# Kernel tuning notes

Hardware: AMD Instinct MI355X
Metric: run time of the kernel (lower is better)

Reference implementation:

```python
import jax, jax.numpy as jnp
import numpy as np
import math

NUM_HEADS = 8

def _ln(x, g, b, eps=1e-5):
    mu = x.mean(-1, keepdims=True)
    var = ((x - mu) ** 2).mean(-1, keepdims=True)
    return (x - mu) / jnp.sqrt(var + eps) * g + b

def setup_inputs() -> dict:
    key = jax.random.key(0)
    ks = jax.random.split(key, 10)
    B, Nq, Nk, dQ, dK, dV = 16, 1024, 1024, 512, 512, 512
    s = 0.05  # small init so the double-exp in masked_softmax stays finite
    Q = jax.random.normal(ks[0], (B, Nq, dQ), jnp.float32)
    K = jax.random.normal(ks[1], (B, Nk, dK), jnp.float32)
    Qm = (jax.random.uniform(ks[2], (B, Nq, 1)) < 0.9).astype(jnp.float32)
    Km = (jax.random.uniform(ks[3], (B, Nk, 1)) < 0.9).astype(jnp.float32)
    Wq = jax.random.normal(ks[4], (dQ, dV), jnp.float32) * s
    Wk = jax.random.normal(ks[5], (dK, dV), jnp.float32) * s
    Wv = jax.random.normal(ks[6], (dK, dV), jnp.float32) * s
    Wo = jax.random.normal(ks[7], (dV, dV), jnp.float32) * s
    bq = jnp.zeros((dV,), jnp.float32); bk = jnp.zeros((dV,), jnp.float32)
    bv = jnp.zeros((dV,), jnp.float32); bo = jnp.zeros((dV,), jnp.float32)
    g0 = jnp.ones((dV,), jnp.float32); b0 = jnp.zeros((dV,), jnp.float32)
    g1 = jnp.ones((dV,), jnp.float32); b1 = jnp.zeros((dV,), jnp.float32)
    return {"Q": Q, "K": K, "Qm": Qm, "Km": Km,
            "Wq": Wq, "bq": bq, "Wk": Wk, "bk": bk, "Wv": Wv, "bv": bv,
            "Wo": Wo, "bo": bo, "g0": g0, "b0": b0, "g1": g1, "b1": b1}

def reference(Q, K, Qm, Km, Wq, bq, Wk, bk, Wv, bv, Wo, bo, g0, b0, g1, b1):
    B, Nq, _ = Q.shape
    Nk = K.shape[1]
    dV = Wq.shape[1]
    h = NUM_HEADS
    dh = dV // h
    # projections + feature masking (Qm/Km broadcast over feature dim)
    Qp = (Q @ Wq + bq) * Qm          # [B,Nq,dV]
    Kp = (K @ Wk + bk) * Km          # [B,Nk,dV]
    V  = K @ Wv + bv                 # [B,Nk,dV]
    # head split: torch.cat(split(dh,2),0) == head-major [h,B,N,dh]
    Qh = Qp.reshape(B, Nq, h, dh).transpose(2, 0, 1, 3)
    Kh = Kp.reshape(B, Nk, h, dh).transpose(2, 0, 1, 3)
    Vh = V.reshape(B, Nk, h, dh).transpose(2, 0, 1, 3)
    S = jnp.einsum('hbqd,hbkd->hbqk', Qh, Kh) / math.sqrt(dV)
    # faithful masked_softmax: exp applied twice (Km branch then Qm branch)
    X = jnp.exp(S) * Km[:, :, 0][None, :, None, :]   # [h,B,Nq,Nk]
    X = jnp.exp(X) * Qm[:, :, 0][None, :, :, None]
    A = X / (X.sum(-1, keepdims=True) + 1e-8)
    O = Qh + jnp.einsum('hbqk,hbkd->hbqd', A, Vh)    # residual in head space
    O = O.transpose(1, 2, 0, 3).reshape(B, Nq, dV)   # merge heads back
    O = _ln(O, g0, b0)
    O = O + jax.nn.relu(O @ Wo + bo)
    return _ln(O, g1, b1)
```

## Files before the change

### kernel.cpp

```cpp
#include <hip/hip_runtime.h>
#include <hip/hip_bf16.h>
#include <cstdint>


typedef __bf16 bf16;
typedef __bf16 bf16x4 __attribute__((ext_vector_type(4)));
typedef __bf16 bf16x8 __attribute__((ext_vector_type(8)));
typedef float f32x4 __attribute__((ext_vector_type(4)));

#define MFMA16(a, b, c) __builtin_amdgcn_mfma_f32_16x16x32_bf16((a), (b), (c), 0, 0, 0)

#if __has_builtin(__builtin_amdgcn_exp2f)
#define EXP2F(x) __builtin_amdgcn_exp2f(x)
#else
#define EXP2F(x) exp2f(x)
#endif

static __device__ __forceinline__ void async_lds16(const bf16* g, bf16* l) {
  __builtin_amdgcn_global_load_lds(
      (__attribute__((address_space(1))) void*)(void*)g,
      (__attribute__((address_space(3))) void*)l,
      16, 0, 0);
}

static __device__ __forceinline__ void swz512(int id, long& rowBase, int& colBase) {
  colBase = ((id >> 3) & 3) * 128;
  rowBase = (long)((id & 7) + 8 * (id >> 5)) * 128;
}

struct ConvArgs {
  const float* src[10];
  bf16* dst[10];
  int n[10];
};

__global__ __launch_bounds__(256) void prep(
    const float* __restrict__ Wq, const float* __restrict__ Wk,
    const float* __restrict__ Wv, const float* __restrict__ Wo,
    bf16* __restrict__ Tq, bf16* __restrict__ Tk,
    bf16* __restrict__ Tv, bf16* __restrict__ To, ConvArgs ca) {
  __shared__ bf16 t[64][72];
  const int id = blockIdx.x;
  const int tid = threadIdx.x;
  if (id < 256) {
    const int bx = id & 7, by = (id >> 3) & 7, bz = id >> 6;
    const float* src;
    bf16* dst;
    switch (bz) {
      case 0: src = Wq; dst = Tq; break;
      case 1: src = Wk; dst = Tk; break;
      case 2: src = Wv; dst = Tv; break;
      default: src = Wo; dst = To; break;
    }
    const int n0 = bx * 64;
    const int k0 = by * 64;
    for (int c = tid; c < 512; c += 256) {
      const int row = c >> 3, col = (c & 7) * 8;
      const float* sp = src + (size_t)(k0 + row) * 512 + n0 + col;
      const f32x4 a = *(const f32x4*)sp;
      const f32x4 b = *(const f32x4*)(sp + 4);
      bf16x8 v;
#pragma unroll
      for (int j = 0; j < 4; ++j) { v[j] = (bf16)a[j]; v[j + 4] = (bf16)b[j]; }
      *(bf16x8*)(&t[row][col]) = v;
    }
    __syncthreads();
    for (int c = tid; c < 512; c += 256) {
      const int row = c >> 3, col8 = (c & 7) * 8;
      bf16x8 v;
#pragma unroll
      for (int j = 0; j < 8; ++j) v[j] = t[col8 + j][row];
      *(bf16x8*)(dst + (size_t)(n0 + row) * 512 + k0 + col8) = v;
    }
  } else {
    const int cid = id - 256;
    const int seg = cid >> 3;
    const int n = ca.n[seg];
    const long i = ((long)(cid & 7) * 256 + tid) * 8;
    if (i >= n) return;
    const float* s = ca.src[seg];
    const f32x4 x0 = *(const f32x4*)(s + i);
    const f32x4 x1 = *(const f32x4*)(s + i + 4);
    bf16x8 o;
#pragma unroll
    for (int j = 0; j < 4; ++j) { o[j] = (bf16)x0[j]; o[j + 4] = (bf16)x1[j]; }
    *(bf16x8*)(ca.dst[seg] + i) = o;
  }
}

__global__ __launch_bounds__(256, 2) void gemm512(
    const bf16* __restrict__ A, const bf16* __restrict__ Bt,
    const bf16* __restrict__ bias, const bf16* __restrict__ mask,
    const bf16* __restrict__ resid, bf16* __restrict__ out) {
  __shared__ bf16 sA[128 * 32];
  __shared__ bf16 sB[128 * 32];
  const int tid = threadIdx.x;
  const int lane = tid & 63;
  const int w = tid >> 6;
  const int fm = lane & 15;
  const int fq = lane >> 4;
  long rowBase; int colBase;
  swz512(blockIdx.x, rowBase, colBase);

  f32x4 acc[4][4] = {};

  const int c0 = tid, c1 = tid + 256;
  const int r0 = c0 >> 2, o0 = (c0 & 3) * 8;
  const int r1 = c1 >> 2, o1 = (c1 & 3) * 8;
  const bf16* A0 = A + (rowBase + r0) * 512 + o0;
  const bf16* A1 = A + (rowBase + r1) * 512 + o1;
  const bf16* B0 = Bt + (size_t)(colBase + r0) * 512 + o0;
  const bf16* B1 = Bt + (size_t)(colBase + r1) * 512 + o1;

  const int wr = (w & 1) * 64;
  const int wc = (w >> 1) * 64;

  for (int kt = 0; kt < 16; ++kt) {
    const int k0 = kt * 32;
    __syncthreads();
    async_lds16(A0 + k0, sA + c0 * 8);
    async_lds16(A1 + k0, sA + c1 * 8);
    async_lds16(B0 + k0, sB + c0 * 8);
    async_lds16(B1 + k0, sB + c1 * 8);
    __syncthreads();
    bf16x8 a[4], b[4];
#pragma unroll
    for (int i = 0; i < 4; ++i)
      a[i] = *(const bf16x8*)(sA + (wr + i * 16 + fm) * 32 + fq * 8);
#pragma unroll
    for (int j = 0; j < 4; ++j)
      b[j] = *(const bf16x8*)(sB + (wc + j * 16 + fm) * 32 + fq * 8);
#pragma unroll
    for (int i = 0; i < 4; ++i)
#pragma unroll
      for (int j = 0; j < 4; ++j)
        acc[i][j] = MFMA16(a[i], b[j], acc[i][j]);
  }

#pragma unroll
  for (int i = 0; i < 4; ++i) {
#pragma unroll
    for (int r = 0; r < 4; ++r) {
      const long R = rowBase + wr + i * 16 + fq * 4 + r;
      const float mk = mask ? (float)mask[R] : 1.0f;
      const bf16* resrow = resid ? resid + R * 512 : nullptr;
      bf16* outrow = out + R * 512;
#pragma unroll
      for (int j = 0; j < 4; ++j) {
        const int C = colBase + wc + j * 16 + fm;
        float v = acc[i][j][r] + (float)bias[C];
        if (mask) v *= mk;
        if (resid) v = (float)resrow[C] + fmaxf(v, 0.0f);
        outrow[C] = (bf16)v;
      }
    }
  }
}

__global__ __launch_bounds__(256, 2) void proj_all(
    const float* __restrict__ Qf, const float* __restrict__ Kf,
    const bf16* __restrict__ Tq, const bf16* __restrict__ Tk,
    const bf16* __restrict__ Tv, const bf16* __restrict__ bq,
    const bf16* __restrict__ bk, const bf16* __restrict__ bv,
    const bf16* __restrict__ Qm, const bf16* __restrict__ Km,
    bf16* __restrict__ Qp, bf16* __restrict__ Kp, bf16* __restrict__ Vt) {
  __shared__ bf16 sA[128 * 32];
  __shared__ bf16 sB1[128 * 32];
  __shared__ bf16 sB2[128 * 32];
  const int tid = threadIdx.x;
  const int lane = tid & 63;
  const int w = tid >> 6;
  const int fm = lane & 15;
  const int fq = lane >> 4;
  const int wr = (w & 1) * 64;
  const int wc = (w >> 1) * 64;
  const int c0 = tid, c1 = tid + 256;
  const int r0 = c0 >> 2, o0 = (c0 & 3) * 8;
  const int r1 = c1 >> 2, o1 = (c1 & 3) * 8;

  if (blockIdx.x < 512) {
    long rowBase; int colBase;
    swz512(blockIdx.x, rowBase, colBase);
    f32x4 acc[4][4] = {};
    const float* A0 = Qf + (rowBase + r0) * 512 + o0;
    const float* A1 = Qf + (rowBase + r1) * 512 + o1;
    const bf16* B0 = Tq + (size_t)(colBase + r0) * 512 + o0;
    const bf16* B1 = Tq + (size_t)(colBase + r1) * 512 + o1;

    f32x4 x0 = *(const f32x4*)(A0);
    f32x4 x1 = *(const f32x4*)(A0 + 4);
    f32x4 y0 = *(const f32x4*)(A1);
    f32x4 y1 = *(const f32x4*)(A1 + 4);

    for (int kt = 0; kt < 16; ++kt) {
      __syncthreads();
      async_lds16(B0 + kt * 32, sB1 + c0 * 8);
      async_lds16(B1 + kt * 32, sB1 + c1 * 8);
      {
        bf16x8 va, vb;
#pragma unroll
        for (int j = 0; j < 4; ++j) {
          va[j] = (bf16)x0[j]; va[j + 4] = (bf16)x1[j];
          vb[j] = (bf16)y0[j]; vb[j + 4] = (bf16)y1[j];
        }
        *(bf16x8*)(sA + c0 * 8) = va;
        *(bf16x8*)(sA + c1 * 8) = vb;
      }
      __syncthreads();
      if (kt < 15) {
        const int k1 = kt * 32 + 32;
        x0 = *(const f32x4*)(A0 + k1);
        x1 = *(const f32x4*)(A0 + k1 + 4);
        y0 = *(const f32x4*)(A1 + k1);
        y1 = *(const f32x4*)(A1 + k1 + 4);
      }
      bf16x8 a[4], b[4];
#pragma unroll
      for (int i = 0; i < 4; ++i)
        a[i] = *(const bf16x8*)(sA + (wr + i * 16 + fm) * 32 + fq * 8);
#pragma unroll
      for (int j = 0; j < 4; ++j)
        b[j] = *(const bf16x8*)(sB1 + (wc + j * 16 + fm) * 32 + fq * 8);
#pragma unroll
      for (int i = 0; i < 4; ++i)
#pragma unroll
        for (int j = 0; j < 4; ++j)
          acc[i][j] = MFMA16(a[i], b[j], acc[i][j]);
    }

#pragma unroll
    for (int i = 0; i < 4; ++i) {
#pragma unroll
      for (int r = 0; r < 4; ++r) {
        const long R = rowBase + wr + i * 16 + fq * 4 + r;
        const float mk = (float)Qm[R];
        bf16* outrow = Qp + R * 512;
#pragma unroll
        for (int j = 0; j < 4; ++j) {
          const int C = colBase + wc + j * 16 + fm;
          outrow[C] = (bf16)((acc[i][j][r] + (float)bq[C]) * mk);
        }
      }
    }
  } else {
    long rowBase; int colBase;
    swz512(blockIdx.x - 512, rowBase, colBase);
    f32x4 acck[4][4] = {};
    f32x4 accv[4][4] = {};
    const float* A0 = Kf + (rowBase + r0) * 512 + o0;
    const float* A1 = Kf + (rowBase + r1) * 512 + o1;
    const bf16* Bk0 = Tk + (size_t)(colBase + r0) * 512 + o0;
    const bf16* Bk1 = Tk + (size_t)(colBase + r1) * 512 + o1;
    const bf16* Bv0 = Tv + (size_t)(colBase + r0) * 512 + o0;
    const bf16* Bv1 = Tv + (size_t)(colBase + r1) * 512 + o1;

    f32x4 x0 = *(const f32x4*)(A0);
    f32x4 x1 = *(const f32x4*)(A0 + 4);
    f32x4 y0 = *(const f32x4*)(A1);
    f32x4 y1 = *(const f32x4*)(A1 + 4);

    for (int kt = 0; kt < 16; ++kt) {
      const int k0 = kt * 32;
      __syncthreads();
      async_lds16(Bk0 + k0, sB1 + c0 * 8);
      async_lds16(Bk1 + k0, sB1 + c1 * 8);
      async_lds16(Bv0 + k0, sB2 + c0 * 8);
      async_lds16(Bv1 + k0, sB2 + c1 * 8);
      {
        bf16x8 va, vb;
#pragma unroll
        for (int j = 0; j < 4; ++j) {
          va[j] = (bf16)x0[j]; va[j + 4] = (bf16)x1[j];
          vb[j] = (bf16)y0[j]; vb[j + 4] = (bf16)y1[j];
        }
        *(bf16x8*)(sA + c0 * 8) = va;
        *(bf16x8*)(sA + c1 * 8) = vb;
      }
      __syncthreads();
      if (kt < 15) {
        const int k1 = k0 + 32;
        x0 = *(const f32x4*)(A0 + k1);
        x1 = *(const f32x4*)(A0 + k1 + 4);
        y0 = *(const f32x4*)(A1 + k1);
        y1 = *(const f32x4*)(A1 + k1 + 4);
      }
      bf16x8 a[4], b[4], bv2[4];
#pragma unroll
      for (int i = 0; i < 4; ++i)
        a[i] = *(const bf16x8*)(sA + (wr + i * 16 + fm) * 32 + fq * 8);
#pragma unroll
      for (int j = 0; j < 4; ++j) {
        b[j] = *(const bf16x8*)(sB1 + (wc + j * 16 + fm) * 32 + fq * 8);
        bv2[j] = *(const bf16x8*)(sB2 + (wc + j * 16 + fm) * 32 + fq * 8);
      }
#pragma unroll
      for (int i = 0; i < 4; ++i)
#pragma unroll
        for (int j = 0; j < 4; ++j) {
          acck[i][j] = MFMA16(a[i], b[j], acck[i][j]);
          accv[i][j] = MFMA16(a[i], bv2[j], accv[i][j]);
        }
    }

    const int bidx = (int)(rowBase >> 10);
#pragma unroll
    for (int i = 0; i < 4; ++i) {
#pragma unroll
      for (int r = 0; r < 4; ++r) {
        const long R = rowBase + wr + i * 16 + fq * 4 + r;
        const float mk = (float)Km[R];
        bf16* outrow = Kp + R * 512;
#pragma unroll
        for (int j = 0; j < 4; ++j) {
          const int C = colBase + wc + j * 16 + fm;
          outrow[C] = (bf16)((acck[i][j][r] + (float)bk[C]) * mk);
        }
      }
      const int kkb = (int)(rowBase & 1023) + wr + i * 16 + fq * 4;
#pragma unroll
      for (int j = 0; j < 4; ++j) {
        const int C = colBase + wc + j * 16 + fm;
        const float bvc = (float)bv[C];
        bf16x4 pv;
#pragma unroll
        for (int r = 0; r < 4; ++r) pv[r] = (bf16)(accv[i][j][r] + bvc);
        bf16* dst =
            Vt + ((size_t)(bidx * 8 + (C >> 6)) * 64 + (C & 63)) * 1024 + kkb;
        *(bf16x4*)((void*)dst) = pv;
      }
    }
  }
}

__global__ __launch_bounds__(256, 4) void attn_kernel(
    bf16* __restrict__ Qp, const bf16* __restrict__ Kp,
    const bf16* __restrict__ Vt, const bf16* __restrict__ Qm,
    const bf16* __restrict__ Km) {
  __shared__ bf16 sK[64][72];
  __shared__ bf16 sVt[64][72];
  __shared__ bf16 sX[4][32][72];
  __shared__ float sKl[64];
  __shared__ float sL[4][32];

  const int tid = threadIdx.x;
  const int lane = tid & 63;
  const int w = tid >> 6;
  const int fm = lane & 15;
  const int fq = lane >> 4;
  const int id = blockIdx.x;
  const int bh = id & 127;
  const int q0 = (id >> 7) * 128;
  const int b = bh >> 3;
  const int hh = bh & 7;
  const int rot = (id >> 3) & 15;

  bf16* Qbase = Qp + ((long)b * 1024 + q0) * 512 + hh * 64;
  float qm_lane[2];
  qm_lane[0] = (float)Qm[(long)b * 1024 + q0 + w * 32 + fm];
  qm_lane[1] = (float)Qm[(long)b * 1024 + q0 + w * 32 + 16 + fm];

  bf16x8 qf[2][2];
#pragma unroll
  for (int u = 0; u < 2; ++u)
#pragma unroll
    for (int ks = 0; ks < 2; ++ks)
      qf[u][ks] = *(const bf16x8*)(Qbase + (long)(w * 32 + u * 16 + fm) * 512 +
                                   ks * 32 + fq * 8);

  f32x4 acc_o[2][4] = {};
  float l_lane[2] = {0.f, 0.f};
  const float c1 = 0.063758715f;
  const float LOG2E = 1.4426950408889634f;

  const bf16* Vthead = Vt + ((long)b * 8 + hh) * 64 * 1024;
  const bf16* Kbb = Kp + (long)b * 1024 * 512 + hh * 64;
  const bf16* Kmb = Km + (long)b * 1024;

  for (int kt = 0; kt < 16; ++kt) {
    const int kk0 = ((kt + rot) & 15) * 64;
    __syncthreads();
    const bf16* Kbase = Kbb + (long)kk0 * 512;
    for (int c = tid; c < 512; c += 256) {
      const int row = c >> 3, col = (c & 7) * 8;
      *(bf16x8*)(&sK[row][col]) = *(const bf16x8*)(Kbase + (long)row * 512 + col);
      *(bf16x8*)(&sVt[row][col]) =
          *(const bf16x8*)(Vthead + (long)row * 1024 + kk0 + col);
    }
    if (tid < 64) sKl[tid] = (float)Kmb[kk0 + tid] * LOG2E;
    __syncthreads();

    f32x4 s_acc[2][4] = {};
#pragma unroll
    for (int ks = 0; ks < 2; ++ks)
#pragma unroll
      for (int t = 0; t < 4; ++t) {
        const bf16x8 kf = *(const bf16x8*)(&sK[t * 16 + fm][ks * 32 + fq * 8]);
        s_acc[0][t] = MFMA16(kf, qf[0][ks], s_acc[0][t]);
        s_acc[1][t] = MFMA16(kf, qf[1][ks], s_acc[1][t]);
      }
#pragma unroll
    for (int u = 0; u < 2; ++u)
#pragma unroll
      for (int t = 0; t < 4; ++t) {
        const f32x4 kml4 = *(const f32x4*)(&sKl[t * 16 + fq * 4]);
        bf16x4 xp;
#pragma unroll
        for (int r = 0; r < 4; ++r) {
          const float e1 = EXP2F(s_acc[u][t][r] * c1);
          const float y = EXP2F(e1 * kml4[r]);
          l_lane[u] += y;
          xp[r] = (bf16)y;
        }
        *(bf16x4*)((void*)&sX[w][u * 16 + fm][t * 16 + fq * 4]) = xp;
      }
#pragma unroll
    for (int ks = 0; ks < 2; ++ks) {
      const bf16x8 xf0 = *(const bf16x8*)(&sX[w][fm][ks * 32 + fq * 8]);
      const bf16x8 xf1 = *(const bf16x8*)(&sX[w][16 + fm][ks * 32 + fq * 8]);
#pragma unroll
      for (int t = 0; t < 4; ++t) {
        const bf16x8 vf = *(const bf16x8*)(&sVt[t * 16 + fm][ks * 32 + fq * 8]);
        acc_o[0][t] = MFMA16(xf0, vf, acc_o[0][t]);
        acc_o[1][t] = MFMA16(xf1, vf, acc_o[1][t]);
      }
    }
  }

#pragma unroll
  for (int u = 0; u < 2; ++u) {
    l_lane[u] += __shfl_xor(l_lane[u], 16);
    l_lane[u] += __shfl_xor(l_lane[u], 32);
    if (fq == 0) sL[w][u * 16 + fm] = l_lane[u];
  }
  __syncthreads();

#pragma unroll
  for (int u = 0; u < 2; ++u) {
#pragma unroll
    for (int t = 0; t < 4; ++t) {
#pragma unroll
      for (int r = 0; r < 4; ++r) {
        const int qr = w * 32 + u * 16 + fq * 4 + r;
        const int dc = t * 16 + fm;
        const float qm_r = __shfl(qm_lane[u], fq * 4 + r, 64);
        const float li = 1.0f / (qm_r * sL[w][u * 16 + fq * 4 + r] + 1e-8f);
        const float val =
            (float)Qbase[(long)qr * 512 + dc] + qm_r * acc_o[u][t][r] * li;
        Qbase[(long)qr * 512 + dc] = (bf16)val;
      }
    }
  }
}

__global__ __launch_bounds__(256) void lnorm(
    const bf16* __restrict__ X, const bf16* __restrict__ g,
    const bf16* __restrict__ bb, bf16* __restrict__ out) {
  const int row = blockIdx.x * 4 + (threadIdx.x >> 6);
  const int lane = threadIdx.x & 63;
  const bf16x8 v = *(const bf16x8*)(X + (size_t)row * 512 + lane * 8);
  float x[8], s = 0.f, ss = 0.f;
#pragma unroll
  for (int j = 0; j < 8; ++j) {
    x[j] = (float)v[j];
    s += x[j];
    ss += x[j] * x[j];
  }
#pragma unroll
  for (int m = 1; m < 64; m <<= 1) {
    s += __shfl_xor(s, m);
    ss += __shfl_xor(ss, m);
  }
  const float mean = s * (1.0f / 512.0f);
  const float var = ss * (1.0f / 512.0f) - mean * mean;
  const float rstd = 1.0f / sqrtf(var + 1e-5f);
  const bf16x8 gv = *(const bf16x8*)(g + lane * 8);
  const bf16x8 bv = *(const bf16x8*)(bb + lane * 8);
  bf16x8 o;
#pragma unroll
  for (int j = 0; j < 8; ++j)
    o[j] = (bf16)((x[j] - mean) * rstd * (float)gv[j] + (float)bv[j]);
  *(bf16x8*)(out + (size_t)row * 512 + lane * 8) = o;
}

__global__ __launch_bounds__(256) void lnorm_out(
    const bf16* __restrict__ X, const bf16* __restrict__ g,
    const bf16* __restrict__ bb, float* __restrict__ out) {
  const int row = blockIdx.x * 4 + (threadIdx.x >> 6);
  const int lane = threadIdx.x & 63;
  const bf16x8 v = *(const bf16x8*)(X + (size_t)row * 512 + lane * 8);
  float x[8], s = 0.f, ss = 0.f;
#pragma unroll
  for (int j = 0; j < 8; ++j) {
    x[j] = (float)v[j];
    s += x[j];
    ss += x[j] * x[j];
  }
#pragma unroll
  for (int m = 1; m < 64; m <<= 1) {
    s += __shfl_xor(s, m);
    ss += __shfl_xor(ss, m);
  }
  const float mean = s * (1.0f / 512.0f);
  const float var = ss * (1.0f / 512.0f) - mean * mean;
  const float rstd = 1.0f / sqrtf(var + 1e-5f);
  const bf16x8 gv = *(const bf16x8*)(g + lane * 8);
  const bf16x8 bv = *(const bf16x8*)(bb + lane * 8);
  f32x4 a, c;
#pragma unroll
  for (int j = 0; j < 4; ++j) {
    a[j] = (x[j] - mean) * rstd * (float)gv[j] + (float)bv[j];
    c[j] = (x[j + 4] - mean) * rstd * (float)gv[j + 4] + (float)bv[j + 4];
  }
  float* fo = out + (size_t)row * 512 + lane * 8;
  *(f32x4*)fo = a;
  *(f32x4*)(fo + 4) = c;
}

extern "C" void kernel_launch(void* const* d_in, const int* in_sizes, int n_in,
                              void* d_out, int out_size, void* d_ws, size_t ws_size,
                              hipStream_t stream) {
  (void)in_sizes; (void)n_in; (void)out_size; (void)ws_size;
  const float* Q = (const float*)d_in[0];
  const float* K = (const float*)d_in[1];

  bf16* ws = (bf16*)d_ws;
  const long W2 = 512L * 512;
  const long MN = 16384L * 512;
  bf16* Tq = ws;
  bf16* Tk = Tq + W2;
  bf16* Tv = Tk + W2;
  bf16* To = Tv + W2;
  bf16* sm = To + W2;
  bf16* cQm = sm + 8 * 512;
  bf16* cKm = cQm + 16384;
  bf16* Qp = cKm + 16384;
  bf16* Kp = Qp + MN;
  bf16* Vt = (bf16*)d_out + MN;

  bf16* cbq = sm + 0 * 512;
  bf16* cbk = sm + 1 * 512;
  bf16* cbv = sm + 2 * 512;
  bf16* cbo = sm + 3 * 512;
  bf16* cg0 = sm + 4 * 512;
  bf16* cb0 = sm + 5 * 512;
  bf16* cg1 = sm + 6 * 512;
  bf16* cb1 = sm + 7 * 512;

  ConvArgs ca;
  ca.src[0] = (const float*)d_in[2];  ca.dst[0] = cQm; ca.n[0] = 16384;
  ca.src[1] = (const float*)d_in[3];  ca.dst[1] = cKm; ca.n[1] = 16384;
  ca.src[2] = (const float*)d_in[5];  ca.dst[2] = cbq; ca.n[2] = 512;
  ca.src[3] = (const float*)d_in[7];  ca.dst[3] = cbk; ca.n[3] = 512;
  ca.src[4] = (const float*)d_in[9];  ca.dst[4] = cbv; ca.n[4] = 512;
  ca.src[5] = (const float*)d_in[11]; ca.dst[5] = cbo; ca.n[5] = 512;
  ca.src[6] = (const float*)d_in[12]; ca.dst[6] = cg0; ca.n[6] = 512;
  ca.src[7] = (const float*)d_in[13]; ca.dst[7] = cb0; ca.n[7] = 512;
  ca.src[8] = (const float*)d_in[14]; ca.dst[8] = cg1; ca.n[8] = 512;
  ca.src[9] = (const float*)d_in[15]; ca.dst[9] = cb1; ca.n[9] = 512;

  prep<<<336, 256, 0, stream>>>(
      (const float*)d_in[4], (const float*)d_in[6],
      (const float*)d_in[8], (const float*)d_in[10], Tq, Tk, Tv, To, ca);

  proj_all<<<1024, 256, 0, stream>>>(Q, K, Tq, Tk, Tv, cbq, cbk, cbv,
                                     cQm, cKm, Qp, Kp, Vt);

  attn_kernel<<<1024, 256, 0, stream>>>(Qp, Kp, Vt, cQm, cKm);

  lnorm<<<4096, 256, 0, stream>>>(Qp, cg0, cb0, Qp);
  gemm512<<<512, 256, 0, stream>>>(Qp, To, cbo, nullptr, Qp, Kp);
  lnorm_out<<<4096, 256, 0, stream>>>(Kp, cg1, cb1, (float*)d_out);
}
```

Measured before the change: 285.6 us.

## Double-buffer K/V tiles with async LDS loads and XOR-swizzled layout

```diff
diff --git a/kernel.cpp b/kernel.cpp
--- a/kernel.cpp
+++ b/kernel.cpp
@@ -308,38 +308,42 @@
 #pragma unroll
       for (int r = 0; r < 4; ++r) {
         const long R = rowBase + wr + i * 16 + fq * 4 + r;
+        const int rs = (int)(R & 7) << 3;
         const float mk = (float)Km[R];
         bf16* outrow = Kp + R * 512;
 #pragma unroll
         for (int j = 0; j < 4; ++j) {
           const int C = colBase + wc + j * 16 + fm;
-          outrow[C] = (bf16)((acck[i][j][r] + (float)bk[C]) * mk);
+          const int Cs = (C & ~63) | ((C & 63) ^ rs);
+          outrow[Cs] = (bf16)((acck[i][j][r] + (float)bk[C]) * mk);
         }
       }
       const int kkb = (int)(rowBase & 1023) + wr + i * 16 + fq * 4;
 #pragma unroll
       for (int j = 0; j < 4; ++j) {
         const int C = colBase + wc + j * 16 + fm;
+        const int ds = (C & 7) << 3;
+        const int kks = (kkb & ~63) | ((kkb & 63) ^ ds);
         const float bvc = (float)bv[C];
         bf16x4 pv;
 #pragma unroll
         for (int r = 0; r < 4; ++r) pv[r] = (bf16)(accv[i][j][r] + bvc);
         bf16* dst =
-            Vt + ((size_t)(bidx * 8 + (C >> 6)) * 64 + (C & 63)) * 1024 + kkb;
+            Vt + ((size_t)(bidx * 8 + (C >> 6)) * 64 + (C & 63)) * 1024 + kks;
         *(bf16x4*)((void*)dst) = pv;
       }
     }
   }
 }
 
-__global__ __launch_bounds__(256, 4) void attn_kernel(
+__global__ __launch_bounds__(256, 3) void attn_kernel(
     bf16* __restrict__ Qp, const bf16* __restrict__ Kp,
     const bf16* __restrict__ Vt, const bf16* __restrict__ Qm,
     const bf16* __restrict__ Km) {
-  __shared__ bf16 sK[64][72];
-  __shared__ bf16 sVt[64][72];
+  __shared__ bf16 sK[2][64][64];
+  __shared__ bf16 sVt[2][64][64];
   __shared__ bf16 sX[4][32][72];
-  __shared__ float sKl[64];
+  __shared__ bf16 sKm[1024];
   __shared__ float sL[4][32];
 
   const int tid = threadIdx.x;
@@ -370,60 +374,87 @@
   f32x4 acc_o[2][4] = {};
   float l_lane[2] = {0.f, 0.f};
   const float c1 = 0.063758715f;
-  const float LOG2E = 1.4426950408889634f;
+  const float C2 = 0.5287663729448977f;
 
   const bf16* Vthead = Vt + ((long)b * 8 + hh) * 64 * 1024;
   const bf16* Kbb = Kp + (long)b * 1024 * 512 + hh * 64;
   const bf16* Kmb = Km + (long)b * 1024;
 
+  const int srow = tid >> 3;
+  const int scol = (tid & 7) * 8;
+  const int xsw = (fm & 7) << 3;
+
+  {
+    const int kk0 = (rot & 15) * 64;
+    const bf16* Kb0 = Kbb + (long)kk0 * 512;
+    async_lds16(Kb0 + (long)srow * 512 + scol, &sK[0][0][0] + tid * 8);
+    async_lds16(Kb0 + (long)(srow + 32) * 512 + scol,
+                &sK[0][0][0] + 2048 + tid * 8);
+    async_lds16(Vthead + (long)srow * 1024 + kk0 + scol, &sVt[0][0][0] + tid * 8);
+    async_lds16(Vthead + (long)(srow + 32) * 1024 + kk0 + scol,
+                &sVt[0][0][0] + 2048 + tid * 8);
+    *(bf16x4*)(&sKm[tid * 4]) = *(const bf16x4*)(Kmb + tid * 4);
+  }
+  __syncthreads();
+
   for (int kt = 0; kt < 16; ++kt) {
-    const int kk0 = ((kt + rot) & 15) * 64;
-    __syncthreads();
-    const bf16* Kbase = Kbb + (long)kk0 * 512;
-    for (int c = tid; c < 512; c += 256) {
-      const int row = c >> 3, col = (c & 7) * 8;
-      *(bf16x8*)(&sK[row][col]) = *(const bf16x8*)(Kbase + (long)row * 512 + col);
-      *(bf16x8*)(&sVt[row][col]) =
-          *(const bf16x8*)(Vthead + (long)row * 1024 + kk0 + col);
-    }
-    if (tid < 64) sKl[tid] = (float)Kmb[kk0 + tid] * LOG2E;
-    __syncthreads();
+    const int cur = kt & 1;
+    if (kt < 15) {
+      const int kk1 = ((kt + 1 + rot) & 15) * 64;
+      const bf16* Kb1 = Kbb + (long)kk1 * 512;
+      bf16* dK = &sK[cur ^ 1][0][0];
+      bf16* dV = &sVt[cur ^ 1][0][0];
+      async_lds16(Kb1 + (long)srow * 512 + scol, dK + tid * 8);
+      async_lds16(Kb1 + (long)(srow + 32) * 512 + scol, dK + 2048 + tid * 8);
+      async_lds16(Vthead + (long)srow * 1024 + kk1 + scol, dV + tid * 8);
+      async_lds16(Vthead + (long)(srow + 32) * 1024 + kk1 + scol,
+                  dV + 2048 + tid * 8);
+    }
+    const int kkT = ((kt + rot) & 15) * 64;
 
     f32x4 s_acc[2][4] = {};
 #pragma unroll
-    for (int ks = 0; ks < 2; ++ks)
+    for (int ks = 0; ks < 2; ++ks) {
+      const int kc = (ks * 32 + fq * 8) ^ xsw;
 #pragma unroll
       for (int t = 0; t < 4; ++t) {
-        const bf16x8 kf = *(const bf16x8*)(&sK[t * 16 + fm][ks * 32 + fq * 8]);
+        const bf16x8 kf = *(const bf16x8*)(&sK[cur][t * 16 + fm][kc]);
         s_acc[0][t] = MFMA16(kf, qf[0][ks], s_acc[0][t]);
         s_acc[1][t] = MFMA16(kf, qf[1][ks], s_acc[1][t]);
       }
-#pragma unroll
-    for (int u = 0; u < 2; ++u)
-#pragma unroll
-      for (int t = 0; t < 4; ++t) {
-        const f32x4 kml4 = *(const f32x4*)(&sKl[t * 16 + fq * 4]);
+    }
+#pragma unroll
+    for (int t = 0; t < 4; ++t) {
+      const bf16x4 km4 = *(const bf16x4*)(&sKm[kkT + t * 16 + fq * 4]);
+      float kmf[4];
+#pragma unroll
+      for (int r = 0; r < 4; ++r) kmf[r] = (float)km4[r];
+#pragma unroll
+      for (int u = 0; u < 2; ++u) {
         bf16x4 xp;
 #pragma unroll
         for (int r = 0; r < 4; ++r) {
-          const float e1 = EXP2F(s_acc[u][t][r] * c1);
-          const float y = EXP2F(e1 * kml4[r]);
+          const float e1L = EXP2F(fmaf(s_acc[u][t][r], c1, C2));
+          const float y = EXP2F(e1L * kmf[r]);
           l_lane[u] += y;
           xp[r] = (bf16)y;
         }
         *(bf16x4*)((void*)&sX[w][u * 16 + fm][t * 16 + fq * 4]) = xp;
       }
+    }
 #pragma unroll
     for (int ks = 0; ks < 2; ++ks) {
+      const int kc = (ks * 32 + fq * 8) ^ xsw;
       const bf16x8 xf0 = *(const bf16x8*)(&sX[w][fm][ks * 32 + fq * 8]);
       const bf16x8 xf1 = *(const bf16x8*)(&sX[w][16 + fm][ks * 32 + fq * 8]);
 #pragma unroll
       for (int t = 0; t < 4; ++t) {
-        const bf16x8 vf = *(const bf16x8*)(&sVt[t * 16 + fm][ks * 32 + fq * 8]);
+        const bf16x8 vf = *(const bf16x8*)(&sVt[cur][t * 16 + fm][kc]);
         acc_o[0][t] = MFMA16(xf0, vf, acc_o[0][t]);
         acc_o[1][t] = MFMA16(xf1, vf, acc_o[1][t]);
       }
     }
+    __syncthreads();
   }
 
 #pragma unroll
```

Measured after the change: 281.8 us. About the same (-1.3%).
